# Performance work log

Hardware: AMD Instinct MI355X
Metric: run time of the kernel (lower is better)

## Reference

```python
import jax, jax.numpy as jnp
import numpy as np

B, T, DIM = 2, 2048, 2048
H, KVH = 32, 8
HD = DIM // H            # 64
Q_PER_KV = H // KVH      # 4
ROPE_THETA = 10000.0


def _rope_tables(T, hd, dtype=jnp.float32):
    inv_freq = 1.0 / (ROPE_THETA ** (jnp.arange(0, hd, 2, dtype=jnp.float32) / hd))  # [hd/2]
    ang = jnp.arange(T, dtype=jnp.float32)[:, None] * inv_freq[None, :]              # [T, hd/2]
    return jnp.cos(ang).astype(dtype), jnp.sin(ang).astype(dtype)


def _apply_rope(x, cos, sin):
    # x: [B, T, h, hd]; cos/sin: [T, hd/2] -> complex multiply on (even, odd) pairs
    B_, T_, h, hd = x.shape
    xr = x.reshape(B_, T_, h, hd // 2, 2)
    xe, xo = xr[..., 0], xr[..., 1]
    c = cos[None, :, None, :]
    s = sin[None, :, None, :]
    re = xe * c - xo * s
    ro = xe * s + xo * c
    return jnp.stack([re, ro], axis=-1).reshape(B_, T_, h, hd)


def setup_inputs() -> dict:
    key = jax.random.key(0)
    kx, kq, kk, kv, ko = jax.random.split(key, 5)
    std = 0.02
    x = jax.random.normal(kx, (B, T, DIM), dtype=jnp.float32)
    wq = jax.random.normal(kq, (DIM, H * HD), dtype=jnp.float32) * std
    wk = jax.random.normal(kk, (DIM, KVH * HD), dtype=jnp.float32) * std
    wv = jax.random.normal(kv, (DIM, KVH * HD), dtype=jnp.float32) * std
    wo = jax.random.normal(ko, (H * HD, DIM), dtype=jnp.float32) * std
    freqs_cos, freqs_sin = _rope_tables(T, HD)
    causal = jnp.tril(jnp.ones((T, T), dtype=bool))
    mask = jnp.where(causal, 0.0, -jnp.inf).astype(jnp.float32)[None, None]  # [1,1,T,T]
    return {"x": x, "wq": wq, "wk": wk, "wv": wv, "wo": wo,
            "freqs_cos": freqs_cos, "freqs_sin": freqs_sin, "mask": mask}


def reference(x, wq, wk, wv, wo, freqs_cos, freqs_sin, mask):
    B_, T_, _ = x.shape
    q = (x @ wq).reshape(B_, T_, H, HD)
    k = (x @ wk).reshape(B_, T_, KVH, HD)
    v = (x @ wv).reshape(B_, T_, KVH, HD)
    q = _apply_rope(q, freqs_cos, freqs_sin)
    k = _apply_rope(k, freqs_cos, freqs_sin)
    # GQA: repeat_interleave KV heads along head dim
    k = jnp.repeat(k, Q_PER_KV, axis=2)
    v = jnp.repeat(v, Q_PER_KV, axis=2)
    q = q.transpose(0, 2, 1, 3)  # [B,H,T,hd]
    k = k.transpose(0, 2, 1, 3)
    v = v.transpose(0, 2, 1, 3)
    scale = HD ** -0.5
    scores = jnp.einsum('bhqd,bhkd->bhqk', q, k) * scale + mask
    probs = jax.nn.softmax(scores.astype(jnp.float32), axis=-1).astype(q.dtype)
    out = jnp.einsum('bhqk,bhkd->bhqd', probs, v)
    out = out.transpose(0, 2, 1, 3).reshape(B_, T_, H * HD)
    return out @ wo
```

## Files before the change

### kernel.cpp

```cpp
#include <hip/hip_runtime.h>
#include <stdint.h>

typedef __bf16 bf16;
typedef __attribute__((ext_vector_type(8))) __bf16 bf16x8;
typedef __attribute__((ext_vector_type(4))) __bf16 bf16x4;
typedef __attribute__((ext_vector_type(4))) float f32x4;
typedef __attribute__((ext_vector_type(16))) float f32x16;
typedef __attribute__((ext_vector_type(4))) unsigned short us4;

constexpr int B_   = 2;
constexpr int T_   = 2048;
constexpr int DIM_ = 2048;
constexpr int H_   = 32;
constexpr int KVH_ = 8;
constexpr int HD_  = 64;
constexpr int BT_ROWS = B_ * T_;
constexpr int NQKV = H_*HD_ + 2*KVH_*HD_;
constexpr int KOFF = H_*HD_;
constexpr int VOFF = H_*HD_ + KVH_*HD_;

#define DEV __device__ __forceinline__

DEV void gload16(const void* g, void* l) {
  __builtin_amdgcn_global_load_lds((const __attribute__((address_space(1))) void*)g,
                                   (__attribute__((address_space(3))) void*)l,
                                   16, 0, 0);
}

__global__ void prep_kernel(const float* __restrict__ x,
                            const float* __restrict__ wq, const float* __restrict__ wk,
                            const float* __restrict__ wv, const float* __restrict__ wo,
                            const float* __restrict__ fc, const float* __restrict__ fs,
                            bf16* __restrict__ xb, bf16* __restrict__ wT,
                            bf16* __restrict__ woT,
                            float* __restrict__ fcT, float* __restrict__ fsT) {
  const int id = blockIdx.x;
  const int tid = threadIdx.y * 32 + threadIdx.x;
  if (id < 8192) {
    int gid = id * 256 + tid;
    float4 f = ((const float4*)x)[gid];
    bf16x4 o;
    o[0] = (bf16)f.x; o[1] = (bf16)f.y; o[2] = (bf16)f.z; o[3] = (bf16)f.w;
    ((bf16x4*)xb)[gid] = o;
    return;
  }
  __shared__ float tile[32][33];
  int td = id - 8192;
  int tx = threadIdx.x, ty = threadIdx.y;
  if (td < 10240) {
    const float* in; bf16* out; int C, bid;
    if (td < 4096)      { in = wq; out = wT;               C = 2048; bid = td; }
    else if (td < 5120) { in = wk; out = wT + 2048*2048;   C = 512;  bid = td - 4096; }
    else if (td < 6144) { in = wv; out = wT + 2560*2048;   C = 512;  bid = td - 5120; }
    else                { in = wo; out = woT;              C = 2048; bid = td - 6144; }
    const int R = 2048;
    int ct = C / 32;
    int bx = bid % ct, by = bid / ct;
#pragma unroll
    for (int i = ty; i < 32; i += 8)
      tile[i][tx] = in[(by*32 + i) * C + bx*32 + tx];
    __syncthreads();
#pragma unroll
    for (int i = ty; i < 32; i += 8)
      out[(bx*32 + i) * R + by*32 + tx] = (bf16)tile[tx][i];
  } else {
    int tt = td - 10240;
    const float* in = (tt >= 64) ? fs : fc;
    float* outf = (tt >= 64) ? fsT : fcT;
    int bid = tt & 63;
#pragma unroll
    for (int i = ty; i < 32; i += 8)
      tile[i][tx] = in[(bid*32 + i) * 32 + tx];
    __syncthreads();
#pragma unroll
    for (int i = ty; i < 32; i += 8)
      outf[i * 2048 + bid*32 + tx] = tile[tx][i];
  }
}

template<int MODE>
__global__ __launch_bounds__(256, MODE == 1 ? 3 : 2)
void gemm_bt(const bf16* __restrict__ A, const bf16* __restrict__ BTm,
             void* __restrict__ Cv, int M, int N, int K,
             const float* __restrict__ fcT, const float* __restrict__ fsT,
             bf16* __restrict__ vt) {
  __shared__ __align__(16) bf16 As[128 * 64];
  __shared__ __align__(16) bf16 Bs[128 * 64];
  const int nbn = N >> 7;
  const int bm = blockIdx.x / nbn, bn = blockIdx.x % nbn;
  const int tid = threadIdx.x;
  const int w = tid >> 6, l = tid & 63;
  const int wr = w >> 1, wc = w & 1;
  const int lr = l & 31;
  const int hi = l >> 5;
  const int crow = l >> 3;
  const int cch  = (l & 7) ^ crow;

  f32x16 acc[2][2];
#pragma unroll
  for (int i = 0; i < 2; ++i)
#pragma unroll
    for (int j = 0; j < 2; ++j) acc[i][j] = 0.f;

  const bf16* ap[4];
  const bf16* bp[4];
#pragma unroll
  for (int i = 0; i < 4; ++i) {
    int row = (w*4 + i) * 8 + crow;
    ap[i] = A   + (long)(bm*128 + row) * K + cch*8;
    bp[i] = BTm + (long)(bn*128 + row) * K + cch*8;
  }
  int aoff[4][2], boff[4][2];
#pragma unroll
  for (int ks = 0; ks < 4; ++ks)
#pragma unroll
    for (int i = 0; i < 2; ++i) {
      int arow = wr*64 + i*32 + lr;
      int brow = wc*64 + i*32 + lr;
      aoff[ks][i] = arow*64 + (((2*ks + hi) ^ (arow & 7)) << 3);
      boff[ks][i] = brow*64 + (((2*ks + hi) ^ (brow & 7)) << 3);
    }

  for (int k0 = 0; k0 < K; k0 += 64) {
#pragma unroll
    for (int i = 0; i < 4; ++i) {
      gload16(ap[i], &As[(w*4 + i) * 512]);
      gload16(bp[i], &Bs[(w*4 + i) * 512]);
      ap[i] += 64; bp[i] += 64;
    }
    __syncthreads();
#pragma unroll
    for (int ks = 0; ks < 4; ++ks) {
      bf16x8 af[2], bfr[2];
#pragma unroll
      for (int i = 0; i < 2; ++i) af[i]  = *(const bf16x8*)&As[aoff[ks][i]];
#pragma unroll
      for (int j = 0; j < 2; ++j) bfr[j] = *(const bf16x8*)&Bs[boff[ks][j]];
#pragma unroll
      for (int i = 0; i < 2; ++i)
#pragma unroll
        for (int j = 0; j < 2; ++j)
          acc[i][j] = __builtin_amdgcn_mfma_f32_32x32x16_bf16(af[i], bfr[j], acc[i][j], 0, 0, 0);
    }
    __syncthreads();
  }

  const int row0 = bm*128 + wr*64, col0 = bn*128 + wc*64;
  if (MODE == 0) {
#pragma unroll
    for (int i = 0; i < 2; ++i)
#pragma unroll
      for (int j = 0; j < 2; ++j)
#pragma unroll
        for (int reg = 0; reg < 16; ++reg) {
          int rr = row0 + i*32 + (reg & 3) + 8*(reg >> 2) + 4*hi;
          int cc = col0 + j*32 + lr;
          ((float*)Cv)[(long)rr * N + cc] = acc[i][j][reg];
        }
  } else {
    if (col0 < VOFF) {
      const float sgn = (lr & 1) ? 1.f : -1.f;
#pragma unroll
      for (int i = 0; i < 2; ++i) {
        const int tb0 = ((row0 + i*32) & (T_ - 1)) + 4*hi;
#pragma unroll
        for (int j = 0; j < 2; ++j) {
          const int cc = col0 + j*32 + lr;
          const float qsc = (col0 + j*32 < KOFF) ? 0.18033688f : 1.0f;
          const int p0 = (cc & 63) >> 1;
          const float* fct = fcT + p0*2048 + tb0;
          const float* fst = fsT + p0*2048 + tb0;
#pragma unroll
          for (int q = 0; q < 4; ++q) {
            float4 c4 = *(const float4*)(fct + 8*q);
            float4 s4 = *(const float4*)(fst + 8*q);
#pragma unroll
            for (int r = 0; r < 4; ++r) {
              float v = acc[i][j][q*4 + r];
              float other = __shfl_xor(v, 1);
              float cse = (&c4.x)[r], sse = (&s4.x)[r];
              float out = fmaf(sgn * other, sse, v * cse) * qsc;
              const int rr = row0 + i*32 + r + 8*q + 4*hi;
              ((bf16*)Cv)[(long)rr * N + cc] = (bf16)out;
            }
          }
        }
      }
    } else {
      const int bglob = row0 >> 11;
#pragma unroll
      for (int i = 0; i < 2; ++i)
#pragma unroll
        for (int j = 0; j < 2; ++j) {
          const int vo = col0 + j*32 + lr - VOFF;
          const long vbase = (long)((bglob*KVH_ + (vo >> 6))*HD_ + (vo & 63)) * T_;
#pragma unroll
          for (int q = 0; q < 4; ++q) {
            bf16x4 pk;
#pragma unroll
            for (int r = 0; r < 4; ++r) pk[r] = (bf16)acc[i][j][q*4 + r];
            const int t = ((row0 + i*32) & (T_ - 1)) + 8*q + 4*hi;
            *(bf16x4*)&vt[vbase + t] = pk;
          }
        }
    }
  }
}

__global__ __launch_bounds__(512, 6)
void attn_kernel(const bf16* __restrict__ qkvb, const bf16* __restrict__ vt,
                 bf16* __restrict__ att) {
  const int o = blockIdx.x;
  const int xcd = o & 7, s = o >> 3;
  const int bh = xcd * 8 + (s & 7);
  const int qt = 15 - (s >> 3);
  const int h = bh & 31, b = bh >> 5;
  const int kvh = h >> 2;
  const int tid = threadIdx.x, w = tid >> 6, l = tid & 63;
  const int ln = l & 15, g = l >> 4;

  __shared__ __align__(16) bf16 Ks[2][4096];
  __shared__ __align__(16) bf16 Vs[2][4096];
  __shared__ __align__(16) bf16 pl[8][16][76];

  const int srow = tid >> 3;
  const int sch  = (tid & 7) ^ (srow & 7);
  const bf16* kg = qkvb + (long)(b*T_ + srow) * NQKV + KOFF + kvh*HD_ + sch*8;
  const bf16* vg = vt + (long)((b*KVH_ + kvh) * HD_ + srow) * T_ + sch*8;
  const int ldsoff = tid * 8;

  const int qrow = (w & 3)*16 + ln;
  float maskadd[4][4];
#pragma unroll
  for (int c = 0; c < 4; ++c)
#pragma unroll
    for (int r = 0; r < 4; ++r)
      maskadd[c][r] = (c*16 + g*4 + r > qrow) ? -1e38f : 0.f;

  bf16x8 onesf;
  {
    const bf16 ov = (ln == 0) ? (bf16)1.0f : (bf16)0.0f;
#pragma unroll
    for (int i = 0; i < 8; ++i) onesf[i] = ov;
  }

  const int qbase = qt * 128;
  const int nt = qt * 2 + 2;
  const int myNt = nt - 1 + (w >> 2);

  const int q0 = qbase + w*16;
  const long qb = (long)(b*T_ + q0 + ln) * NQKV + h*HD_;
  bf16x8 qf0 = *(const bf16x8*)&qkvb[qb + g*8];
  bf16x8 qf1 = *(const bf16x8*)&qkvb[qb + 32 + g*8];

  f32x4 oacc[4], osum;
#pragma unroll
  for (int d = 0; d < 4; ++d) oacc[d] = 0.f;
  osum = 0.f;

  gload16(kg, &Ks[0][ldsoff]);
  gload16(vg, &Vs[0][ldsoff]);
  __syncthreads();

  int cur = 0;
  for (int kt = 0; kt < nt; ++kt) {
    if (kt + 1 < nt) {
      const int k1 = (kt + 1) * 64;
      gload16(kg + (long)k1 * NQKV, &Ks[cur^1][ldsoff]);
      gload16(vg + k1,              &Vs[cur^1][ldsoff]);
    }
    if (kt < myNt) {
      f32x4 sv[4];
      __builtin_amdgcn_s_setprio(1);
#pragma unroll
      for (int c = 0; c < 4; ++c) {
        const int krow = c*16 + ln, sw = krow & 7;
        bf16x8 kf0 = *(const bf16x8*)&Ks[cur][krow*64 + (( g    ^ sw) << 3)];
        bf16x8 kf1 = *(const bf16x8*)&Ks[cur][krow*64 + (((g+4) ^ sw) << 3)];
        f32x4 z = 0.f;
        z     = __builtin_amdgcn_mfma_f32_16x16x32_bf16(kf0, qf0, z, 0, 0, 0);
        sv[c] = __builtin_amdgcn_mfma_f32_16x16x32_bf16(kf1, qf1, z, 0, 0, 0);
      }
      __builtin_amdgcn_s_setprio(0);

      if (kt == myNt - 1) {
#pragma unroll
        for (int c = 0; c < 4; ++c)
#pragma unroll
          for (int r = 0; r < 4; ++r)
            sv[c][r] += maskadd[c][r];
      }

#pragma unroll
      for (int c = 0; c < 4; ++c) {
        bf16x4 pk;
#pragma unroll
        for (int r = 0; r < 4; ++r)
          pk[r] = (bf16)exp2f(sv[c][r]);
        *(bf16x4*)&pl[w][ln][c*16 + g*4] = pk;
      }

      bf16x8 pa0 = *(const bf16x8*)&pl[w][ln][g*8];
      bf16x8 pa1 = *(const bf16x8*)&pl[w][ln][32 + g*8];

      __builtin_amdgcn_s_setprio(1);
#pragma unroll
      for (int d = 0; d < 4; ++d) {
        const int vrow = d*16 + ln, sw = vrow & 7;
        bf16x8 vf0 = *(const bf16x8*)&Vs[cur][vrow*64 + (( g    ^ sw) << 3)];
        bf16x8 vf1 = *(const bf16x8*)&Vs[cur][vrow*64 + (((g+4) ^ sw) << 3)];
        oacc[d] = __builtin_amdgcn_mfma_f32_16x16x32_bf16(vf0, pa0, oacc[d], 0, 0, 0);
        oacc[d] = __builtin_amdgcn_mfma_f32_16x16x32_bf16(vf1, pa1, oacc[d], 0, 0, 0);
      }
      osum = __builtin_amdgcn_mfma_f32_16x16x32_bf16(onesf, pa0, osum, 0, 0, 0);
      osum = __builtin_amdgcn_mfma_f32_16x16x32_bf16(onesf, pa1, osum, 0, 0, 0);
      __builtin_amdgcn_s_setprio(0);
    }
    __syncthreads();
    cur ^= 1;
  }

  const float lsum = __shfl(osum[0], ln);
  const float inv = 1.f / lsum;
  const long ob = (long)(b*T_ + q0 + ln) * DIM_ + h*HD_;
#pragma unroll
  for (int d = 0; d < 4; ++d) {
    bf16x4 ov;
#pragma unroll
    for (int r = 0; r < 4; ++r) ov[r] = (bf16)(oacc[d][r] * inv);
    *(bf16x4*)&att[ob + d*16 + g*4] = ov;
  }
}

extern "C" void kernel_launch(void* const* d_in, const int* in_sizes, int n_in,
                              void* d_out, int out_size, void* d_ws, size_t ws_size,
                              hipStream_t stream) {
  const float* x  = (const float*)d_in[0];
  const float* wq = (const float*)d_in[1];
  const float* wk = (const float*)d_in[2];
  const float* wv = (const float*)d_in[3];
  const float* wo = (const float*)d_in[4];
  const float* fc = (const float*)d_in[5];
  const float* fs = (const float*)d_in[6];

  char* ws = (char*)d_ws;
  bf16* xb   = (bf16*)(ws);
  bf16* wT   = (bf16*)(ws + 16777216);
  bf16* woT  = (bf16*)(ws + 29360128);
  bf16* qkvb = (bf16*)(ws + 37748736);
  bf16* vtb  = (bf16*)(ws + 62914560);
  bf16* att  = (bf16*)(ws + 67108864);
  float* fcT = (float*)(ws + 67108864);
  float* fsT = fcT + 32*2048;

  dim3 tb(32, 8);
  prep_kernel<<<18560, tb, 0, stream>>>(x, wq, wk, wv, wo, fc, fs, xb, wT, woT, fcT, fsT);

  gemm_bt<1><<<(BT_ROWS/128) * (NQKV/128), 256, 0, stream>>>(
      xb, wT, qkvb, BT_ROWS, NQKV, DIM_, fcT, fsT, vtb);

  attn_kernel<<<1024, 512, 0, stream>>>(qkvb, vtb, att);

  gemm_bt<0><<<(BT_ROWS/128) * (DIM_/128), 256, 0, stream>>>(
      att, woT, d_out, BT_ROWS, DIM_, DIM_, nullptr, nullptr, nullptr);
}
```

Measured before the change: 188.1 us.

## Unroll attention loop by two with explicit vmcnt waits and precomputed LDS offsets

Restructures the attention K/V loop into a two-tile unrolled body with compile-time buffer indices. Both buffers are prefetched up front. __syncthreads is replaced by raw s_barrier plus explicit s_waitcnt vmcnt counts, so the next tile's global-to-LDS loads can stay in flight across the barrier. LDS addresses are precomputed as byte offsets to cut per-iteration address arithmetic. The hand-written waitcnt accounting is fragile: a wrong count could read stale LDS data.

Result: slower. 207.5 us (+10.3%).

```diff
diff --git a/kernel.cpp b/kernel.cpp
--- a/kernel.cpp
+++ b/kernel.cpp
@@ -207,6 +207,58 @@
   }
 }
 
+template<int CUR>
+DEV void attn_tile(int kt, int myNt,
+                   const char* ksB, const char* vsB, char* plB,
+                   int kb0, int kb1, int pw0, int pr0,
+                   const bf16x8& qf0, const bf16x8& qf1,
+                   const float (&maskadd)[4][4], const bf16x8& onesf,
+                   f32x4 (&oacc)[4], f32x4& osum) {
+  if (kt >= myNt) return;
+  f32x4 sv[4];
+  __builtin_amdgcn_s_setprio(1);
+#pragma unroll
+  for (int c = 0; c < 4; ++c) {
+    bf16x8 kf0 = *(const bf16x8*)(ksB + CUR*8192 + c*2048 + kb0);
+    bf16x8 kf1 = *(const bf16x8*)(ksB + CUR*8192 + c*2048 + kb1);
+    f32x4 z = {0.f, 0.f, 0.f, 0.f};
+    z     = __builtin_amdgcn_mfma_f32_16x16x32_bf16(kf0, qf0, z, 0, 0, 0);
+    sv[c] = __builtin_amdgcn_mfma_f32_16x16x32_bf16(kf1, qf1, z, 0, 0, 0);
+  }
+  __builtin_amdgcn_s_setprio(0);
+
+  if (kt == myNt - 1) {
+#pragma unroll
+    for (int c = 0; c < 4; ++c)
+#pragma unroll
+      for (int r = 0; r < 4; ++r)
+        sv[c][r] += maskadd[c][r];
+  }
+
+#pragma unroll
+  for (int c = 0; c < 4; ++c) {
+    bf16x4 pk;
+#pragma unroll
+    for (int r = 0; r < 4; ++r)
+      pk[r] = (bf16)exp2f(sv[c][r]);
+    *(bf16x4*)(plB + pw0 + c*32) = pk;
+  }
+  bf16x8 pa0 = *(const bf16x8*)(plB + pr0);
+  bf16x8 pa1 = *(const bf16x8*)(plB + pr0 + 64);
+
+  __builtin_amdgcn_s_setprio(1);
+#pragma unroll
+  for (int d = 0; d < 4; ++d) {
+    bf16x8 vf0 = *(const bf16x8*)(vsB + CUR*8192 + d*2048 + kb0);
+    bf16x8 vf1 = *(const bf16x8*)(vsB + CUR*8192 + d*2048 + kb1);
+    oacc[d] = __builtin_amdgcn_mfma_f32_16x16x32_bf16(vf0, pa0, oacc[d], 0, 0, 0);
+    oacc[d] = __builtin_amdgcn_mfma_f32_16x16x32_bf16(vf1, pa1, oacc[d], 0, 0, 0);
+  }
+  osum = __builtin_amdgcn_mfma_f32_16x16x32_bf16(onesf, pa0, osum, 0, 0, 0);
+  osum = __builtin_amdgcn_mfma_f32_16x16x32_bf16(onesf, pa1, osum, 0, 0, 0);
+  __builtin_amdgcn_s_setprio(0);
+}
+
 __global__ __launch_bounds__(512, 6)
 void attn_kernel(const bf16* __restrict__ qkvb, const bf16* __restrict__ vt,
                  bf16* __restrict__ att) {
@@ -229,6 +281,14 @@
   const bf16* vg = vt + (long)((b*KVH_ + kvh) * HD_ + srow) * T_ + sch*8;
   const int ldsoff = tid * 8;
 
+  const int kb0 = (ln << 7) | (((g    ) ^ (ln & 7)) << 4);
+  const int kb1 = (ln << 7) | (((g + 4) ^ (ln & 7)) << 4);
+  const int pw0 = (w*16 + ln) * 152 + g*8;
+  const int pr0 = (w*16 + ln) * 152 + g*16;
+  const char* ksB = (const char*)&Ks[0][0];
+  const char* vsB = (const char*)&Vs[0][0];
+  char* plB = (char*)&pl[0][0][0];
+
   const int qrow = (w & 3)*16 + ln;
   float maskadd[4][4];
 #pragma unroll
@@ -260,64 +320,42 @@
 
   gload16(kg, &Ks[0][ldsoff]);
   gload16(vg, &Vs[0][ldsoff]);
-  __syncthreads();
-
-  int cur = 0;
-  for (int kt = 0; kt < nt; ++kt) {
-    if (kt + 1 < nt) {
-      const int k1 = (kt + 1) * 64;
-      gload16(kg + (long)k1 * NQKV, &Ks[cur^1][ldsoff]);
-      gload16(vg + k1,              &Vs[cur^1][ldsoff]);
-    }
-    if (kt < myNt) {
-      f32x4 sv[4];
-      __builtin_amdgcn_s_setprio(1);
-#pragma unroll
-      for (int c = 0; c < 4; ++c) {
-        const int krow = c*16 + ln, sw = krow & 7;
-        bf16x8 kf0 = *(const bf16x8*)&Ks[cur][krow*64 + (( g    ^ sw) << 3)];
-        bf16x8 kf1 = *(const bf16x8*)&Ks[cur][krow*64 + (((g+4) ^ sw) << 3)];
-        f32x4 z = 0.f;
-        z     = __builtin_amdgcn_mfma_f32_16x16x32_bf16(kf0, qf0, z, 0, 0, 0);
-        sv[c] = __builtin_amdgcn_mfma_f32_16x16x32_bf16(kf1, qf1, z, 0, 0, 0);
+  gload16(kg + (long)64 * NQKV, &Ks[1][ldsoff]);
+  gload16(vg + 64,              &Vs[1][ldsoff]);
+  asm volatile("s_waitcnt vmcnt(2)" ::: "memory");
+  __builtin_amdgcn_sched_barrier(0);
+  __builtin_amdgcn_s_barrier();
+
+  for (int kt = 0; kt < nt; kt += 2) {
+    attn_tile<0>(kt, myNt, ksB, vsB, plB, kb0, kb1, pw0, pr0,
+                 qf0, qf1, maskadd, onesf, oacc, osum);
+    __builtin_amdgcn_s_barrier();
+    if (kt + 2 < nt) {
+      gload16(kg + (long)(kt+2)*64*NQKV, &Ks[0][ldsoff]);
+      gload16(vg + (kt+2)*64,            &Vs[0][ldsoff]);
+      asm volatile("s_waitcnt vmcnt(2)" ::: "memory");
+    } else {
+      asm volatile("s_waitcnt vmcnt(0)" ::: "memory");
+    }
+    __builtin_amdgcn_sched_barrier(0);
+    __builtin_amdgcn_s_barrier();
+
+    attn_tile<1>(kt + 1, myNt, ksB, vsB, plB, kb0, kb1, pw0, pr0,
+                 qf0, qf1, maskadd, onesf, oacc, osum);
+    __builtin_amdgcn_s_barrier();
+    if (kt + 3 < nt) {
+      gload16(kg + (long)(kt+3)*64*NQKV, &Ks[1][ldsoff]);
+      gload16(vg + (kt+3)*64,            &Vs[1][ldsoff]);
+    }
+    if (kt + 2 < nt) {
+      if (kt + 3 < nt) {
+        asm volatile("s_waitcnt vmcnt(2)" ::: "memory");
+      } else {
+        asm volatile("s_waitcnt vmcnt(0)" ::: "memory");
       }
-      __builtin_amdgcn_s_setprio(0);
-
-      if (kt == myNt - 1) {
-#pragma unroll
-        for (int c = 0; c < 4; ++c)
-#pragma unroll
-          for (int r = 0; r < 4; ++r)
-            sv[c][r] += maskadd[c][r];
-      }
-
-#pragma unroll
-      for (int c = 0; c < 4; ++c) {
-        bf16x4 pk;
-#pragma unroll
-        for (int r = 0; r < 4; ++r)
-          pk[r] = (bf16)exp2f(sv[c][r]);
-        *(bf16x4*)&pl[w][ln][c*16 + g*4] = pk;
-      }
-
-      bf16x8 pa0 = *(const bf16x8*)&pl[w][ln][g*8];
-      bf16x8 pa1 = *(const bf16x8*)&pl[w][ln][32 + g*8];
-
-      __builtin_amdgcn_s_setprio(1);
-#pragma unroll
-      for (int d = 0; d < 4; ++d) {
-        const int vrow = d*16 + ln, sw = vrow & 7;
-        bf16x8 vf0 = *(const bf16x8*)&Vs[cur][vrow*64 + (( g    ^ sw) << 3)];
-        bf16x8 vf1 = *(const bf16x8*)&Vs[cur][vrow*64 + (((g+4) ^ sw) << 3)];
-        oacc[d] = __builtin_amdgcn_mfma_f32_16x16x32_bf16(vf0, pa0, oacc[d], 0, 0, 0);
-        oacc[d] = __builtin_amdgcn_mfma_f32_16x16x32_bf16(vf1, pa1, oacc[d], 0, 0, 0);
-      }
-      osum = __builtin_amdgcn_mfma_f32_16x16x32_bf16(onesf, pa0, osum, 0, 0, 0);
-      osum = __builtin_amdgcn_mfma_f32_16x16x32_bf16(onesf, pa1, osum, 0, 0, 0);
-      __builtin_amdgcn_s_setprio(0);
-    }
-    __syncthreads();
-    cur ^= 1;
+      __builtin_amdgcn_sched_barrier(0);
+      __builtin_amdgcn_s_barrier();
+    }
   }
 
   const float lsum = __shfl(osum[0], ln);
```

## Process two 16-row query tiles per wave in attention with 256-thread blocks

Applied to the files above, without the earlier changes.

Halves the attention block to 4 waves, with each wave now owning 32 query rows (two 16-row MFMA tiles) instead of 16. Each K/V fragment read from LDS is reused across both query tiles, and each thread issues two async loads per tensor per tile. This cuts LDS reads per MFMA and the number of waves sharing the per-tile barrier. In exchange it roughly doubles accumulator and score registers per wave, and occupancy drops to 4 waves per block with launch bounds of 3 blocks.

After: 186.2 us (median of 2 runs). About the same (-1.0%).

```diff
diff --git a/kernel.cpp b/kernel.cpp
--- a/kernel.cpp
+++ b/kernel.cpp
@@ -207,7 +207,7 @@
   }
 }
 
-__global__ __launch_bounds__(512, 6)
+__global__ __launch_bounds__(256, 3)
 void attn_kernel(const bf16* __restrict__ qkvb, const bf16* __restrict__ vt,
                  bf16* __restrict__ att) {
   const int o = blockIdx.x;
@@ -221,7 +221,7 @@
 
   __shared__ __align__(16) bf16 Ks[2][4096];
   __shared__ __align__(16) bf16 Vs[2][4096];
-  __shared__ __align__(16) bf16 pl[8][16][76];
+  __shared__ __align__(16) bf16 pl[4][32][76];
 
   const int srow = tid >> 3;
   const int sch  = (tid & 7) ^ (srow & 7);
@@ -229,13 +229,8 @@
   const bf16* vg = vt + (long)((b*KVH_ + kvh) * HD_ + srow) * T_ + sch*8;
   const int ldsoff = tid * 8;
 
-  const int qrow = (w & 3)*16 + ln;
-  float maskadd[4][4];
-#pragma unroll
-  for (int c = 0; c < 4; ++c)
-#pragma unroll
-    for (int r = 0; r < 4; ++r)
-      maskadd[c][r] = (c*16 + g*4 + r > qrow) ? -1e38f : 0.f;
+  const int qrel0 = (w & 1)*32 + ln;
+  const int qrel1 = qrel0 + 16;
 
   bf16x8 onesf;
   {
@@ -246,40 +241,49 @@
 
   const int qbase = qt * 128;
   const int nt = qt * 2 + 2;
-  const int myNt = nt - 1 + (w >> 2);
-
-  const int q0 = qbase + w*16;
-  const long qb = (long)(b*T_ + q0 + ln) * NQKV + h*HD_;
-  bf16x8 qf0 = *(const bf16x8*)&qkvb[qb + g*8];
-  bf16x8 qf1 = *(const bf16x8*)&qkvb[qb + 32 + g*8];
-
-  f32x4 oacc[4], osum;
-#pragma unroll
-  for (int d = 0; d < 4; ++d) oacc[d] = 0.f;
-  osum = 0.f;
+  const int myNt = qt*2 + 1 + (w >> 1);
+
+  const int q0 = qbase + w*32;
+  const long qb0 = (long)(b*T_ + q0 + ln) * NQKV + h*HD_;
+  const long qb1 = (long)(b*T_ + q0 + 16 + ln) * NQKV + h*HD_;
+  bf16x8 qf0a = *(const bf16x8*)&qkvb[qb0 + g*8];
+  bf16x8 qf0b = *(const bf16x8*)&qkvb[qb0 + 32 + g*8];
+  bf16x8 qf1a = *(const bf16x8*)&qkvb[qb1 + g*8];
+  bf16x8 qf1b = *(const bf16x8*)&qkvb[qb1 + 32 + g*8];
+
+  f32x4 oacc0[4], oacc1[4], osum0, osum1;
+#pragma unroll
+  for (int d = 0; d < 4; ++d) { oacc0[d] = 0.f; oacc1[d] = 0.f; }
+  osum0 = 0.f; osum1 = 0.f;
 
   gload16(kg, &Ks[0][ldsoff]);
+  gload16(kg + (long)32*NQKV, &Ks[0][ldsoff + 2048]);
   gload16(vg, &Vs[0][ldsoff]);
+  gload16(vg + (long)32*T_, &Vs[0][ldsoff + 2048]);
   __syncthreads();
 
   int cur = 0;
   for (int kt = 0; kt < nt; ++kt) {
     if (kt + 1 < nt) {
       const int k1 = (kt + 1) * 64;
-      gload16(kg + (long)k1 * NQKV, &Ks[cur^1][ldsoff]);
-      gload16(vg + k1,              &Vs[cur^1][ldsoff]);
+      gload16(kg + (long)k1 * NQKV,        &Ks[cur^1][ldsoff]);
+      gload16(kg + (long)(k1+32) * NQKV,   &Ks[cur^1][ldsoff + 2048]);
+      gload16(vg + k1,                     &Vs[cur^1][ldsoff]);
+      gload16(vg + (long)32*T_ + k1,       &Vs[cur^1][ldsoff + 2048]);
     }
     if (kt < myNt) {
-      f32x4 sv[4];
+      f32x4 sv0[4], sv1[4];
       __builtin_amdgcn_s_setprio(1);
 #pragma unroll
       for (int c = 0; c < 4; ++c) {
         const int krow = c*16 + ln, sw = krow & 7;
         bf16x8 kf0 = *(const bf16x8*)&Ks[cur][krow*64 + (( g    ^ sw) << 3)];
         bf16x8 kf1 = *(const bf16x8*)&Ks[cur][krow*64 + (((g+4) ^ sw) << 3)];
-        f32x4 z = 0.f;
-        z     = __builtin_amdgcn_mfma_f32_16x16x32_bf16(kf0, qf0, z, 0, 0, 0);
-        sv[c] = __builtin_amdgcn_mfma_f32_16x16x32_bf16(kf1, qf1, z, 0, 0, 0);
+        f32x4 z0 = 0.f, z1 = 0.f;
+        z0     = __builtin_amdgcn_mfma_f32_16x16x32_bf16(kf0, qf0a, z0, 0, 0, 0);
+        sv0[c] = __builtin_amdgcn_mfma_f32_16x16x32_bf16(kf1, qf0b, z0, 0, 0, 0);
+        z1     = __builtin_amdgcn_mfma_f32_16x16x32_bf16(kf0, qf1a, z1, 0, 0, 0);
+        sv1[c] = __builtin_amdgcn_mfma_f32_16x16x32_bf16(kf1, qf1b, z1, 0, 0, 0);
       }
       __builtin_amdgcn_s_setprio(0);
 
@@ -287,21 +291,29 @@
 #pragma unroll
         for (int c = 0; c < 4; ++c)
 #pragma unroll
-          for (int r = 0; r < 4; ++r)
-            sv[c][r] += maskadd[c][r];
+          for (int r = 0; r < 4; ++r) {
+            const int krel = c*16 + g*4 + r;
+            sv0[c][r] += (krel > qrel0) ? -1e38f : 0.f;
+            sv1[c][r] += (krel > qrel1) ? -1e38f : 0.f;
+          }
       }
 
 #pragma unroll
       for (int c = 0; c < 4; ++c) {
-        bf16x4 pk;
-#pragma unroll
-        for (int r = 0; r < 4; ++r)
-          pk[r] = (bf16)exp2f(sv[c][r]);
-        *(bf16x4*)&pl[w][ln][c*16 + g*4] = pk;
-      }
-
-      bf16x8 pa0 = *(const bf16x8*)&pl[w][ln][g*8];
-      bf16x8 pa1 = *(const bf16x8*)&pl[w][ln][32 + g*8];
+        bf16x4 pk0, pk1;
+#pragma unroll
+        for (int r = 0; r < 4; ++r) {
+          pk0[r] = (bf16)exp2f(sv0[c][r]);
+          pk1[r] = (bf16)exp2f(sv1[c][r]);
+        }
+        *(bf16x4*)&pl[w][ln][c*16 + g*4]      = pk0;
+        *(bf16x4*)&pl[w][16 + ln][c*16 + g*4] = pk1;
+      }
+
+      bf16x8 pa0a = *(const bf16x8*)&pl[w][ln][g*8];
+      bf16x8 pa0b = *(const bf16x8*)&pl[w][ln][32 + g*8];
+      bf16x8 pa1a = *(const bf16x8*)&pl[w][16 + ln][g*8];
+      bf16x8 pa1b = *(const bf16x8*)&pl[w][16 + ln][32 + g*8];
 
       __builtin_amdgcn_s_setprio(1);
 #pragma unroll
@@ -309,26 +321,44 @@
         const int vrow = d*16 + ln, sw = vrow & 7;
         bf16x8 vf0 = *(const bf16x8*)&Vs[cur][vrow*64 + (( g    ^ sw) << 3)];
         bf16x8 vf1 = *(const bf16x8*)&Vs[cur][vrow*64 + (((g+4) ^ sw) << 3)];
-        oacc[d] = __builtin_amdgcn_mfma_f32_16x16x32_bf16(vf0, pa0, oacc[d], 0, 0, 0);
-        oacc[d] = __builtin_amdgcn_mfma_f32_16x16x32_bf16(vf1, pa1, oacc[d], 0, 0, 0);
-      }
-      osum = __builtin_amdgcn_mfma_f32_16x16x32_bf16(onesf, pa0, osum, 0, 0, 0);
-      osum = __builtin_amdgcn_mfma_f32_16x16x32_bf16(onesf, pa1, osum, 0, 0, 0);
+        oacc0[d] = __builtin_amdgcn_mfma_f32_16x16x32_bf16(vf0, pa0a, oacc0[d], 0, 0, 0);
+        oacc0[d] = __builtin_amdgcn_mfma_f32_16x16x32_bf16(vf1, pa0b, oacc0[d], 0, 0, 0);
+        oacc1[d] = __builtin_amdgcn_mfma_f32_16x16x32_bf16(vf0, pa1a, oacc1[d], 0, 0, 0);
+        oacc1[d] = __builtin_amdgcn_mfma_f32_16x16x32_bf16(vf1, pa1b, oacc1[d], 0, 0, 0);
+      }
+      osum0 = __builtin_amdgcn_mfma_f32_16x16x32_bf16(onesf, pa0a, osum0, 0, 0, 0);
+      osum0 = __builtin_amdgcn_mfma_f32_16x16x32_bf16(onesf, pa0b, osum0, 0, 0, 0);
+      osum1 = __builtin_amdgcn_mfma_f32_16x16x32_bf16(onesf, pa1a, osum1, 0, 0, 0);
+      osum1 = __builtin_amdgcn_mfma_f32_16x16x32_bf16(onesf, pa1b, osum1, 0, 0, 0);
       __builtin_amdgcn_s_setprio(0);
     }
     __syncthreads();
     cur ^= 1;
   }
 
-  const float lsum = __shfl(osum[0], ln);
-  const float inv = 1.f / lsum;
-  const long ob = (long)(b*T_ + q0 + ln) * DIM_ + h*HD_;
-#pragma unroll
-  for (int d = 0; d < 4; ++d) {
-    bf16x4 ov;
-#pragma unroll
-    for (int r = 0; r < 4; ++r) ov[r] = (bf16)(oacc[d][r] * inv);
-    *(bf16x4*)&att[ob + d*16 + g*4] = ov;
+  {
+    const float lsum = __shfl(osum0[0], ln);
+    const float inv = 1.f / lsum;
+    const long ob = (long)(b*T_ + q0 + ln) * DIM_ + h*HD_;
+#pragma unroll
+    for (int d = 0; d < 4; ++d) {
+      bf16x4 ov;
+#pragma unroll
+      for (int r = 0; r < 4; ++r) ov[r] = (bf16)(oacc0[d][r] * inv);
+      *(bf16x4*)&att[ob + d*16 + g*4] = ov;
+    }
+  }
+  {
+    const float lsum = __shfl(osum1[0], ln);
+    const float inv = 1.f / lsum;
+    const long ob = (long)(b*T_ + q0 + 16 + ln) * DIM_ + h*HD_;
+#pragma unroll
+    for (int d = 0; d < 4; ++d) {
+      bf16x4 ov;
+#pragma unroll
+      for (int r = 0; r < 4; ++r) ov[r] = (bf16)(oacc1[d][r] * inv);
+      *(bf16x4*)&att[ob + d*16 + g*4] = ov;
+    }
   }
 }
 
@@ -359,7 +389,7 @@
   gemm_bt<1><<<(BT_ROWS/128) * (NQKV/128), 256, 0, stream>>>(
       xb, wT, qkvb, BT_ROWS, NQKV, DIM_, fcT, fsT, vtb);
 
-  attn_kernel<<<1024, 512, 0, stream>>>(qkvb, vtb, att);
+  attn_kernel<<<1024, 256, 0, stream>>>(qkvb, vtb, att);
 
   gemm_bt<0><<<(BT_ROWS/128) * (DIM_/128), 256, 0, stream>>>(
       att, woT, d_out, BT_ROWS, DIM_, DIM_, nullptr, nullptr, nullptr);
```
